# Kernel optimization log

Hardware: AMD Instinct MI355X
Metric: run time of the kernel (lower is better)

## Reference

```python
import jax, jax.numpy as jnp
import numpy as np

N = 50000      # nodes
E = 800000     # edges (avg degree 16)
IN = 64        # input_dim
OUT = 64       # output_dim
T = 4          # num_node_types
R = 5          # num_relations
H = 4          # heads
D = OUT // H   # head_dim = 16
LN_EPS = 1e-5


def setup_inputs() -> dict:
    key = jax.random.key(0)
    ks = jax.random.split(key, 20)
    s = 0.02
    glorot = np.sqrt(6.0 / (D + D))
    inp = {
        "x": jax.random.normal(ks[0], (N, IN), jnp.float32),
        "node_types": jax.random.randint(ks[1], (N,), 0, T, jnp.int32),
        "edge_index": jax.random.randint(ks[2], (2, E), 0, N, jnp.int64),
        "edge_types": jax.random.randint(ks[3], (E,), 0, R, jnp.int32),
        # per-node-type linear layers, stacked: [T, in, out] / [T, out]
        "Wk": jax.random.normal(ks[4], (T, IN, OUT), jnp.float32) * s,
        "bk": jnp.zeros((T, OUT), jnp.float32),
        "Wq": jax.random.normal(ks[5], (T, IN, OUT), jnp.float32) * s,
        "bq": jnp.zeros((T, OUT), jnp.float32),
        "Wv": jax.random.normal(ks[6], (T, IN, OUT), jnp.float32) * s,
        "bv": jnp.zeros((T, OUT), jnp.float32),
        "Wa": jax.random.normal(ks[7], (T, OUT, OUT), jnp.float32) * s,
        "ba": jnp.zeros((T, OUT), jnp.float32),
        # per-node-type LayerNorm params
        "ln_g": jnp.ones((T, OUT), jnp.float32),
        "ln_b": jnp.zeros((T, OUT), jnp.float32),
        # relation params
        "rel_pri": jnp.ones((R, H), jnp.float32),
        "rel_att": jax.random.uniform(ks[8], (R, H, D, D), jnp.float32, -glorot, glorot),
        "rel_msg": jax.random.uniform(ks[9], (R, H, D, D), jnp.float32, -glorot, glorot),
        "skip_weights": jnp.ones((T,), jnp.float32),
    }
    return inp


def _typed_linear(x, W, b, node_types):
    # per-node-type linear: compute all T projections ([T,N,out] is small: T*N*out)
    # then select each node's row by its type.
    all_t = jnp.einsum('ni,tio->tno', x, W)                       # [T,N,out]
    sel = jnp.take_along_axis(all_t, node_types[None, :, None], axis=0)[0]
    return sel + b[node_types]                                     # [N,out]


def _hgt_forward(x, node_types, edge_index, edge_types,
                 Wk, bk, Wq, bq, Wv, bv, Wa, ba, ln_g, ln_b,
                 rel_pri, rel_att, rel_msg, skip_weights):
    src = edge_index[0]   # j (source)
    tgt = edge_index[1]   # i (target, segment id for softmax / aggregation)

    Kn = _typed_linear(x, Wk, bk, node_types)  # [N,out]
    Qn = _typed_linear(x, Wq, bq, node_types)
    Vn = _typed_linear(x, Wv, bv, node_types)

    q = Qn[tgt].reshape(E, H, D)   # [E,H,D]
    k = Kn[src].reshape(E, H, D)
    v = Vn[src].reshape(E, H, D)

    # relation-specific transforms: k' = k @ rel_att[r], v' = v @ rel_msg[r]
    # loop over the small fixed set of relations (avoids [E,H,D,D] gather)
    k2 = jnp.zeros_like(k)
    v2 = jnp.zeros_like(v)
    for r in range(R):
        m = (edge_types == r)[:, None, None]
        k2 = k2 + jnp.where(m, jnp.einsum('ehd,hdf->ehf', k, rel_att[r]), 0.0)
        v2 = v2 + jnp.where(m, jnp.einsum('ehd,hdf->ehf', v, rel_msg[r]), 0.0)

    scale = np.float32(np.sqrt(D))
    att = (q * k2).sum(-1) * rel_pri[edge_types] / scale           # [E,H]

    # segment softmax over edges sharing a target node
    amax = jax.ops.segment_max(att, tgt, num_segments=N)           # [N,H]
    ex = jnp.exp(att - amax[tgt])
    den = jax.ops.segment_sum(ex, tgt, num_segments=N)             # [N,H]
    attw = ex / den[tgt]                                           # [E,H]

    msg = (v2 * attw[..., None]).reshape(E, OUT)                   # [E,out]
    agg = jax.ops.segment_sum(msg, tgt, num_segments=N)            # [N,out]

    # update: gelu -> per-type linear -> skip mix -> per-type LayerNorm
    # (dropout omitted: eval mode)
    out_g = jax.nn.gelu(agg, approximate=False)
    trans = _typed_linear(out_g, Wa, ba, node_types)               # [N,out]
    sk = jax.nn.sigmoid(skip_weights)[node_types][:, None]         # [N,1]
    res = trans * sk + x * (1.0 - sk)
    mu = res.mean(-1, keepdims=True)
    var = res.var(-1, keepdims=True)
    res = (res - mu) / jnp.sqrt(var + LN_EPS)
    return res * ln_g[node_types] + ln_b[node_types]


def reference(x, node_types, edge_index, edge_types,
              Wk, bk, Wq, bq, Wv, bv, Wa, ba, ln_g, ln_b,
              rel_pri, rel_att, rel_msg, skip_weights):
    return _hgt_forward(x, node_types, edge_index, edge_types,
                        Wk, bk, Wq, bq, Wv, bv, Wa, ba, ln_g, ln_b,
                        rel_pri, rel_att, rel_msg, skip_weights)
```

## Files before the change

### kernel.cpp

```cpp
#include <hip/hip_runtime.h>
#include <math.h>

#define N_NODES 50000
#define N_EDGES 800000

#define OFF_KV     0
#define OFF_QN     3200000
#define OFF_AGG    6400000
#define OFF_CNT    9600000
#define OFF_SMALL  10400000
#define OFF_BTH    10400100
#define OFF_ORDER  10401000
#define OFF_COL    10452000

__device__ __forceinline__ float gelu_f(float a) {
    return 0.5f * a * (1.0f + erff(a * 0.70710678118654752f));
}

__device__ __forceinline__ unsigned pack_kv(float kf, float vf) {
    unsigned ku = __float_as_uint(kf);
    ku = (ku + 0x7FFFu + ((ku >> 16) & 1u)) >> 16;
    unsigned vu = __float_as_uint(vf);
    vu = (vu + 0x7FFFu + ((vu >> 16) & 1u)) & 0xFFFF0000u;
    return vu | ku;
}

__global__ __launch_bounds__(256) void scatter_direct_k(const int* __restrict__ ei,
                                                        const int* __restrict__ et,
                                                        const int* __restrict__ ntype,
                                                        int* __restrict__ cnt,
                                                        int* __restrict__ col,
                                                        int* __restrict__ bth) {
    int e = blockIdx.x * 256 + threadIdx.x;
    int tgt = ei[N_EDGES + e];
    int slot = atomicAdd(&cnt[tgt << 4], 1);
    if (slot < 64)
        col[(tgt << 6) + slot] = ei[e] | (et[e] << 20);
    if (blockIdx.x < 196) {
        __shared__ int wc[4][4];
        int tid = threadIdx.x, w = tid >> 6, lane = tid & 63;
        int i = blockIdx.x * 256 + tid;
        int t = (i < N_NODES) ? ntype[i] : 255;
#pragma unroll
        for (int tt = 0; tt < 4; ++tt) {
            unsigned long long m = __ballot(t == tt);
            if (lane == 0) wc[w][tt] = __popcll(m);
        }
        __syncthreads();
        if (tid < 4)
            bth[tid * 196 + blockIdx.x] = wc[0][tid] + wc[1][tid] + wc[2][tid] + wc[3][tid];
    }
}

__global__ __launch_bounds__(256) void typescan_k(int* __restrict__ bth,
                                                  int* __restrict__ small) {
    int tid = threadIdx.x, wv = tid >> 6, lane = tid & 63;
    __shared__ int tot_s[4];
    __shared__ int noff_s[4];
    int pre[4]; int carry = 0;
#pragma unroll
    for (int c = 0; c < 4; ++c) {
        int b = c * 64 + lane;
        int v = (b < 196) ? bth[wv * 196 + b] : 0;
        int s = v;
#pragma unroll
        for (int o = 1; o < 64; o <<= 1) { int u = __shfl_up(s, o); if (lane >= o) s += u; }
        pre[c] = carry + s - v;
        carry += __shfl(s, 63);
    }
    if (lane == 0) tot_s[wv] = carry;
    __syncthreads();
    if (tid == 0) {
        int o = 0, cb = 0;
#pragma unroll
        for (int k = 0; k < 4; ++k) {
            small[k] = tot_s[k];
            small[8 + k] = o; noff_s[k] = o;
            small[16 + k] = cb;
            o += tot_s[k]; cb += (tot_s[k] + 63) >> 6;
        }
        small[12] = o; small[20] = cb;
    }
    __syncthreads();
    int noff = noff_s[wv];
#pragma unroll
    for (int c = 0; c < 4; ++c) {
        int b = c * 64 + lane;
        if (b < 196) bth[wv * 196 + b] = noff + pre[c];
    }
}

__global__ __launch_bounds__(256) void order_k(const int* __restrict__ ntype,
                                               const int* __restrict__ bth,
                                               int* __restrict__ order) {
    int tid = threadIdx.x, w = tid >> 6, lane = tid & 63;
    int i = blockIdx.x * 256 + tid;
    __shared__ int wc[4][4];
    int t = (i < N_NODES) ? ntype[i] : 255;
    int myrank = 0;
#pragma unroll
    for (int tt = 0; tt < 4; ++tt) {
        unsigned long long m = __ballot(t == tt);
        if (lane == 0) wc[w][tt] = __popcll(m);
        if (t == tt) myrank = __popcll(m & ((1ull << lane) - 1ull));
    }
    __syncthreads();
    if (t < 4) {
        int base = 0;
#pragma unroll
        for (int w2 = 0; w2 < 4; ++w2) if (w2 < w) base += wc[w2][t];
        order[bth[t * 196 + blockIdx.x] + base + myrank] = i;
    }
}

__device__ __forceinline__ void mat16(const float* __restrict__ W,
                                      const float* __restrict__ B,
                                      const float* xs, int lane, int wvu,
                                      float acc[16]) {
    const float* Bp = B + wvu * 16;
#pragma unroll
    for (int c = 0; c < 16; c += 4) {
        float4 b4 = *(const float4*)(Bp + c);
        acc[c] = b4.x; acc[c + 1] = b4.y; acc[c + 2] = b4.z; acc[c + 3] = b4.w;
    }
    const float* Wp = W + wvu * 16;
#pragma unroll 4
    for (int i = 0; i < 64; ++i) {
        float xi = xs[i * 64 + lane];
#pragma unroll
        for (int c = 0; c < 16; c += 4) {
            float4 w4 = *(const float4*)(Wp + i * 64 + c);
            acc[c]     = fmaf(xi, w4.x, acc[c]);
            acc[c + 1] = fmaf(xi, w4.y, acc[c + 1]);
            acc[c + 2] = fmaf(xi, w4.z, acc[c + 2]);
            acc[c + 3] = fmaf(xi, w4.w, acc[c + 3]);
        }
    }
}

__global__ __launch_bounds__(256) void kqv_k(const float* __restrict__ x,
                                             const int* __restrict__ order,
                                             const int* __restrict__ small,
                                             const float* __restrict__ Wk, const float* __restrict__ bk,
                                             const float* __restrict__ Wq, const float* __restrict__ bq,
                                             const float* __restrict__ Wv, const float* __restrict__ bv,
                                             float* __restrict__ Qn,
                                             unsigned* __restrict__ KVu) {
    __shared__ float xs[4096];
    int tid = threadIdx.x, wv = tid >> 6, lane = tid & 63;
    int wid = blockIdx.x;
    int cb1 = small[17], cb2 = small[18], cb3 = small[19], cb4 = small[20];
    if (wid >= cb4) return;
    int t = (wid >= cb1) + (wid >= cb2) + (wid >= cb3);
    int cbt = small[16 + t];
    int noff = small[8 + t], cntt = small[t];
    int pos = noff + (wid - cbt) * 64 + lane;
    int end = noff + cntt;
    bool valid = pos < end;
    int node = order[valid ? pos : end - 1];
    t = __builtin_amdgcn_readfirstlane(t);
    int wvu = __builtin_amdgcn_readfirstlane(wv);

    const float* xr = x + node * 64 + wvu * 16;
    float4 a0 = *(const float4*)(xr + 0), a1 = *(const float4*)(xr + 4),
           a2 = *(const float4*)(xr + 8), a3 = *(const float4*)(xr + 12);
    float st[16] = { a0.x, a0.y, a0.z, a0.w, a1.x, a1.y, a1.z, a1.w,
                     a2.x, a2.y, a2.z, a2.w, a3.x, a3.y, a3.z, a3.w };
#pragma unroll
    for (int k = 0; k < 16; ++k) xs[(wvu * 16 + k) * 64 + lane] = st[k];
    __syncthreads();

    float aq[16];
    mat16(Wq + t * 4096, bq + t * 64, xs, lane, wvu, aq);
    if (valid) {
        float* Op = Qn + node * 64 + wvu * 16;
#pragma unroll
        for (int c = 0; c < 16; c += 4) {
            float4 o4 = { aq[c], aq[c + 1], aq[c + 2], aq[c + 3] };
            *(float4*)(Op + c) = o4;
        }
    }
    float ak[16], av[16];
    mat16(Wk + t * 4096, bk + t * 64, xs, lane, wvu, ak);
    mat16(Wv + t * 4096, bv + t * 64, xs, lane, wvu, av);
    if (valid) {
        unsigned pk[16];
#pragma unroll
        for (int c = 0; c < 16; ++c) pk[c] = pack_kv(ak[c], av[c]);
        uint4* dst = (uint4*)(KVu + node * 64 + wvu * 16);
#pragma unroll
        for (int c = 0; c < 4; ++c)
            dst[c] = *(uint4*)&pk[c * 4];
    }
}

#define BF_LO(u) __uint_as_float((u) << 16)
#define BF_HI(u) __uint_as_float((u) & 0xFFFF0000u)

#define LOADB(CC, AA, BB, T) do {                                          \
    int idx_ = (T) * 4 + g; if (idx_ > deg - 1) idx_ = deg - 1;            \
    int cc_ = __shfl(colv, idx_);                                          \
    (CC) = cc_;                                                            \
    const unsigned* kvp_ = KVu + (unsigned)(cc_ & 0xFFFFF) * 64;           \
    (AA) = *(const uint2*)(kvp_ + 2 * l);                                  \
    (BB) = *(const uint2*)(kvp_ + 32 + 2 * l);                             \
} while (0)

#define COMPUTE(CC, AA, BB, T) do {                                        \
    int rr_ = (CC) >> 20;                                                  \
    const float* qq_ = qp_s + rr_ * 64 + 2 * l;                            \
    float2 qA_ = *(const float2*)qq_;                                      \
    float2 qB_ = *(const float2*)(qq_ + 32);                               \
    float kA0_ = BF_LO((AA).x), vA0_ = BF_HI((AA).x);                      \
    float kA1_ = BF_LO((AA).y), vA1_ = BF_HI((AA).y);                      \
    float kB0_ = BF_LO((BB).x), vB0_ = BF_HI((BB).x);                      \
    float kB1_ = BF_LO((BB).y), vB1_ = BF_HI((BB).y);                      \
    float sA_ = fmaf(kA1_, qA_.y, kA0_ * qA_.x);                           \
    float sB_ = fmaf(kB1_, qB_.y, kB0_ * qB_.x);                           \
    sA_ += __shfl_xor(sA_, 1); sB_ += __shfl_xor(sB_, 1);                  \
    sA_ += __shfl_xor(sA_, 2); sB_ += __shfl_xor(sB_, 2);                  \
    sA_ += __shfl_xor(sA_, 4); sB_ += __shfl_xor(sB_, 4);                  \
    bool act_ = ((T) * 4 + g) < deg;                                       \
    float pA_ = act_ ? __expf(sA_) : 0.0f;                                 \
    float pB_ = act_ ? __expf(sB_) : 0.0f;                                 \
    dnA += pA_; dnB += pB_;                                                \
    _Pragma("unroll")                                                      \
    for (int k_ = 0; k_ < 5; ++k_) {                                       \
        bool mk_ = (rr_ == k_);                                            \
        float pAk_ = mk_ ? pA_ : 0.0f, pBk_ = mk_ ? pB_ : 0.0f;            \
        OA[k_].x = fmaf(pAk_, vA0_, OA[k_].x);                             \
        OA[k_].y = fmaf(pAk_, vA1_, OA[k_].y);                             \
        OB[k_].x = fmaf(pBk_, vB0_, OB[k_].x);                             \
        OB[k_].y = fmaf(pBk_, vB1_, OB[k_].y);                             \
    }                                                                      \
} while (0)

__global__ __launch_bounds__(128) void attn_k(const float* __restrict__ Qn,
                                              const unsigned* __restrict__ KVu,
                                              const int* __restrict__ cnt,
                                              const int* __restrict__ col,
                                              const float* __restrict__ rel_att,
                                              const float* __restrict__ rel_msg,
                                              const float* __restrict__ rel_pri,
                                              float* __restrict__ agg) {
    __shared__ float lds[1408];
    const int tid = threadIdx.x, wv = tid >> 6, lane = tid & 63;
    const int g = lane >> 4, l = lane & 15;
    const int node = blockIdx.x * 2 + wv;
    float* q_s  = lds + wv * 704;
    float* qp_s = q_s + 64;
    float* o_s  = qp_s + 320;

    int deg = cnt[node << 4];
    deg = (deg > 64) ? 64 : deg;
    int colv = col[(node << 6) + lane];
    q_s[lane] = Qn[node * 64 + lane];
    __builtin_amdgcn_wave_barrier();

    const int gb = g * 16;
    float4 qf0 = *(const float4*)(q_s + gb + 0);
    float4 qf1 = *(const float4*)(q_s + gb + 4);
    float4 qf2 = *(const float4*)(q_s + gb + 8);
    float4 qf3 = *(const float4*)(q_s + gb + 12);
#pragma unroll
    for (int r = 0; r < 5; ++r) {
        const float* A = rel_att + ((r * 4 + g) * 16 + l) * 16;
        float4 b0 = *(const float4*)(A + 0), b1 = *(const float4*)(A + 4),
               b2 = *(const float4*)(A + 8), b3 = *(const float4*)(A + 12);
        float acc = b0.x * qf0.x;
        acc = fmaf(b0.y, qf0.y, acc); acc = fmaf(b0.z, qf0.z, acc); acc = fmaf(b0.w, qf0.w, acc);
        acc = fmaf(b1.x, qf1.x, acc); acc = fmaf(b1.y, qf1.y, acc);
        acc = fmaf(b1.z, qf1.z, acc); acc = fmaf(b1.w, qf1.w, acc);
        acc = fmaf(b2.x, qf2.x, acc); acc = fmaf(b2.y, qf2.y, acc);
        acc = fmaf(b2.z, qf2.z, acc); acc = fmaf(b2.w, qf2.w, acc);
        acc = fmaf(b3.x, qf3.x, acc); acc = fmaf(b3.y, qf3.y, acc);
        acc = fmaf(b3.z, qf3.z, acc); acc = fmaf(b3.w, qf3.w, acc);
        qp_s[r * 64 + gb + l] = acc * rel_pri[r * 4 + g] * 0.25f;
    }
    __builtin_amdgcn_wave_barrier();

    if (deg == 0) {
        agg[node * 64 + lane] = 0.0f;
        return;
    }
    int nit = (deg + 3) >> 2;

    float dnA = 0.0f, dnB = 0.0f;
    float2 OA[5], OB[5];
#pragma unroll
    for (int k = 0; k < 5; ++k) { OA[k] = {0.f, 0.f}; OB[k] = {0.f, 0.f}; }

    int c0, c1, c2;
    uint2 A0, B0, A1, B1, A2, B2;
    LOADB(c0, A0, B0, 0);
    LOADB(c1, A1, B1, 1);
    LOADB(c2, A2, B2, 2);

    int t = 0;
    for (;;) {
        COMPUTE(c0, A0, B0, t); if (t + 3 < nit) LOADB(c0, A0, B0, t + 3);
        if (++t >= nit) break;
        COMPUTE(c1, A1, B1, t); if (t + 3 < nit) LOADB(c1, A1, B1, t + 3);
        if (++t >= nit) break;
        COMPUTE(c2, A2, B2, t); if (t + 3 < nit) LOADB(c2, A2, B2, t + 3);
        if (++t >= nit) break;
    }

#pragma unroll
    for (int k = 0; k < 5; ++k) {
        OA[k].x += __shfl_xor(OA[k].x, 16); OA[k].x += __shfl_xor(OA[k].x, 32);
        OA[k].y += __shfl_xor(OA[k].y, 16); OA[k].y += __shfl_xor(OA[k].y, 32);
        OB[k].x += __shfl_xor(OB[k].x, 16); OB[k].x += __shfl_xor(OB[k].x, 32);
        OB[k].y += __shfl_xor(OB[k].y, 16); OB[k].y += __shfl_xor(OB[k].y, 32);
    }
    dnA += __shfl_xor(dnA, 16); dnA += __shfl_xor(dnA, 32);
    dnB += __shfl_xor(dnB, 16); dnB += __shfl_xor(dnB, 32);

    if (g == 0) {
#pragma unroll
        for (int k = 0; k < 5; ++k) {
            *(float2*)(o_s + k * 64 + 2 * l) = OA[k];
            *(float2*)(o_s + k * 64 + 32 + 2 * l) = OB[k];
        }
        if (l == 0) { q_s[0] = dnA; q_s[2] = dnB; }
        if (l == 8) { q_s[1] = dnA; q_s[3] = dnB; }
    }
    __builtin_amdgcn_wave_barrier();

    float F = 0.0f;
#pragma unroll
    for (int k = 0; k < 5; ++k) {
        const float* ob = o_s + k * 64 + gb;
        float4 o0 = *(const float4*)(ob + 0), o1 = *(const float4*)(ob + 4),
               o2 = *(const float4*)(ob + 8), o3 = *(const float4*)(ob + 12);
        const float* M = rel_msg + ((k * 4 + g) * 16) * 16 + l;
        F = fmaf(o0.x, M[0],   F); F = fmaf(o0.y, M[16],  F);
        F = fmaf(o0.z, M[32],  F); F = fmaf(o0.w, M[48],  F);
        F = fmaf(o1.x, M[64],  F); F = fmaf(o1.y, M[80],  F);
        F = fmaf(o1.z, M[96],  F); F = fmaf(o1.w, M[112], F);
        F = fmaf(o2.x, M[128], F); F = fmaf(o2.y, M[144], F);
        F = fmaf(o2.z, M[160], F); F = fmaf(o2.w, M[176], F);
        F = fmaf(o3.x, M[192], F); F = fmaf(o3.y, M[208], F);
        F = fmaf(o3.z, M[224], F); F = fmaf(o3.w, M[240], F);
    }
    float dsel = q_s[g];
    float rd = (dsel > 0.0f) ? (1.0f / dsel) : 0.0f;
    agg[node * 64 + lane] = F * rd;
}

__global__ __launch_bounds__(256) void final_k(const float* __restrict__ x,
                                               const int* __restrict__ order,
                                               const int* __restrict__ small,
                                               const float* __restrict__ agg,
                                               const float* __restrict__ Wa,
                                               const float* __restrict__ ba,
                                               const float* __restrict__ ln_g,
                                               const float* __restrict__ ln_b,
                                               const float* __restrict__ skipw,
                                               float* __restrict__ out) {
    __shared__ float xs[4096];
    __shared__ float res_s[4096];
    int tid = threadIdx.x, wv = tid >> 6, lane = tid & 63;
    int wid = blockIdx.x;
    int cb1 = small[17], cb2 = small[18], cb3 = small[19], cb4 = small[20];
    if (wid >= cb4) return;
    int t = (wid >= cb1) + (wid >= cb2) + (wid >= cb3);
    int cbt = small[16 + t];
    int noff = small[8 + t], cntt = small[t];
    int pos = noff + (wid - cbt) * 64 + lane;
    int end = noff + cntt;
    bool valid = pos < end;
    int node = order[valid ? pos : end - 1];
    t = __builtin_amdgcn_readfirstlane(t);
    int wvu = __builtin_amdgcn_readfirstlane(wv);

    const float* ar = agg + node * 64 + wvu * 16;
    float4 a0 = *(const float4*)(ar + 0), a1 = *(const float4*)(ar + 4),
           a2 = *(const float4*)(ar + 8), a3 = *(const float4*)(ar + 12);
    float st[16] = { gelu_f(a0.x), gelu_f(a0.y), gelu_f(a0.z), gelu_f(a0.w),
                     gelu_f(a1.x), gelu_f(a1.y), gelu_f(a1.z), gelu_f(a1.w),
                     gelu_f(a2.x), gelu_f(a2.y), gelu_f(a2.z), gelu_f(a2.w),
                     gelu_f(a3.x), gelu_f(a3.y), gelu_f(a3.z), gelu_f(a3.w) };
#pragma unroll
    for (int k = 0; k < 16; ++k) xs[(wvu * 16 + k) * 64 + lane] = st[k];
    __syncthreads();

    float acc[16];
    const float* Bp = ba + t * 64 + wvu * 16;
#pragma unroll
    for (int c = 0; c < 16; c += 4) {
        float4 b4 = *(const float4*)(Bp + c);
        acc[c] = b4.x; acc[c + 1] = b4.y; acc[c + 2] = b4.z; acc[c + 3] = b4.w;
    }
    const float* Wp = Wa + t * 4096 + wvu * 16;
#pragma unroll 4
    for (int i = 0; i < 64; ++i) {
        float xi = xs[i * 64 + lane];
#pragma unroll
        for (int c = 0; c < 16; c += 4) {
            float4 w4 = *(const float4*)(Wp + i * 64 + c);
            acc[c]     = fmaf(xi, w4.x, acc[c]);
            acc[c + 1] = fmaf(xi, w4.y, acc[c + 1]);
            acc[c + 2] = fmaf(xi, w4.z, acc[c + 2]);
            acc[c + 3] = fmaf(xi, w4.w, acc[c + 3]);
        }
    }
    float sk = 1.0f / (1.0f + __expf(-skipw[t]));
    float om = 1.0f - sk;
    const float* xrow = x + node * 64 + wvu * 16;
#pragma unroll
    for (int c = 0; c < 16; c += 4) {
        float4 xv = *(const float4*)(xrow + c);
        acc[c]     = acc[c] * sk + xv.x * om;
        acc[c + 1] = acc[c + 1] * sk + xv.y * om;
        acc[c + 2] = acc[c + 2] * sk + xv.z * om;
        acc[c + 3] = acc[c + 3] * sk + xv.w * om;
    }
#pragma unroll
    for (int k = 0; k < 16; ++k) res_s[(wvu * 16 + k) * 64 + lane] = acc[k];
    __syncthreads();

    float sum = 0.0f, ssq = 0.0f;
#pragma unroll
    for (int c = 0; c < 64; ++c) {
        float rv = res_s[c * 64 + lane];
        sum += rv; ssq = fmaf(rv, rv, ssq);
    }
    float mu = sum * (1.0f / 64.0f);
    float var = ssq * (1.0f / 64.0f) - mu * mu;
    float rstd = rsqrtf(var + 1e-5f);
    const float* lg = ln_g + t * 64 + wvu * 16;
    const float* lb = ln_b + t * 64 + wvu * 16;
    if (valid) {
        float* op = out + node * 64 + wvu * 16;
#pragma unroll
        for (int c = 0; c < 16; c += 4) {
            float4 ov;
            ov.x = (acc[c]     - mu) * rstd * lg[c]     + lb[c];
            ov.y = (acc[c + 1] - mu) * rstd * lg[c + 1] + lb[c + 1];
            ov.z = (acc[c + 2] - mu) * rstd * lg[c + 2] + lb[c + 2];
            ov.w = (acc[c + 3] - mu) * rstd * lg[c + 3] + lb[c + 3];
            *(float4*)(op + c) = ov;
        }
    }
}

extern "C" void kernel_launch(void* const* d_in, const int* in_sizes, int n_in,
                              void* d_out, int out_size, void* d_ws, size_t ws_size,
                              hipStream_t stream) {
    const float* x       = (const float*)d_in[0];
    const int*   ntype   = (const int*)d_in[1];
    const int*   ei      = (const int*)d_in[2];
    const int*   et      = (const int*)d_in[3];
    const float* Wk      = (const float*)d_in[4];
    const float* bk      = (const float*)d_in[5];
    const float* Wq      = (const float*)d_in[6];
    const float* bq      = (const float*)d_in[7];
    const float* Wv      = (const float*)d_in[8];
    const float* bv      = (const float*)d_in[9];
    const float* Wa      = (const float*)d_in[10];
    const float* ba      = (const float*)d_in[11];
    const float* ln_g    = (const float*)d_in[12];
    const float* ln_b    = (const float*)d_in[13];
    const float* rel_pri = (const float*)d_in[14];
    const float* rel_att = (const float*)d_in[15];
    const float* rel_msg = (const float*)d_in[16];
    const float* skipw   = (const float*)d_in[17];
    float* out = (float*)d_out;

    float* ws = (float*)d_ws;
    unsigned* KVu = (unsigned*)(ws + OFF_KV);
    float* Qn  = ws + OFF_QN;
    float* agg = ws + OFF_AGG;
    int* cnt   = (int*)(ws + OFF_CNT);
    int* small = (int*)(ws + OFF_SMALL);
    int* bth   = (int*)(ws + OFF_BTH);
    int* order = (int*)(ws + OFF_ORDER);
    int* col   = (int*)(ws + OFF_COL);

    hipMemsetAsync(cnt, 0, 800000 * sizeof(int), stream);
    scatter_direct_k<<<3125, 256, 0, stream>>>(ei, et, ntype, cnt, col, bth);
    typescan_k<<<1, 256, 0, stream>>>(bth, small);
    order_k<<<196, 256, 0, stream>>>(ntype, bth, order);
    kqv_k<<<786, 256, 0, stream>>>(x, order, small, Wk, bk, Wq, bq, Wv, bv, Qn, KVu);
    attn_k<<<25000, 128, 0, stream>>>(Qn, KVu, cnt, col, rel_att, rel_msg, rel_pri, agg);
    final_k<<<786, 256, 0, stream>>>(x, order, small, agg, Wa, ba, ln_g, ln_b, skipw, out);
}
```

Before: 223.1 us.

## Fuse edge scatter into KQV kernel and replace memset with prep kernel

Replaces the hipMemsetAsync of the count array with a small prep kernel that zeroes counts and computes per-block type histograms. The edge scatter is moved out of the first kernel and into the KQV projection launch as extra blocks, so the scatter atomics and the projection run concurrently in one grid. This aims to cut launch overhead and let the latency-bound scatter overlap with compute-bound projection work. The fused kernel reserves 16KB of shared memory even in scatter blocks, which can lower their occupancy.

After: 224.5 us. No clear change (+0.6%).

```diff
diff --git a/kernel.cpp b/kernel.cpp
--- a/kernel.cpp
+++ b/kernel.cpp
@@ -13,6 +13,9 @@
 #define OFF_ORDER  10401000
 #define OFF_COL    10452000
 
+#define SCATTER_BLOCKS 3125
+#define KQV_BLOCKS     786
+
 __device__ __forceinline__ float gelu_f(float a) {
     return 0.5f * a * (1.0f + erff(a * 0.70710678118654752f));
 }
@@ -25,31 +28,27 @@
     return vu | ku;
 }
 
-__global__ __launch_bounds__(256) void scatter_direct_k(const int* __restrict__ ei,
-                                                        const int* __restrict__ et,
-                                                        const int* __restrict__ ntype,
-                                                        int* __restrict__ cnt,
-                                                        int* __restrict__ col,
-                                                        int* __restrict__ bth) {
-    int e = blockIdx.x * 256 + threadIdx.x;
-    int tgt = ei[N_EDGES + e];
-    int slot = atomicAdd(&cnt[tgt << 4], 1);
-    if (slot < 64)
-        col[(tgt << 6) + slot] = ei[e] | (et[e] << 20);
-    if (blockIdx.x < 196) {
-        __shared__ int wc[4][4];
-        int tid = threadIdx.x, w = tid >> 6, lane = tid & 63;
-        int i = blockIdx.x * 256 + tid;
-        int t = (i < N_NODES) ? ntype[i] : 255;
-#pragma unroll
-        for (int tt = 0; tt < 4; ++tt) {
-            unsigned long long m = __ballot(t == tt);
-            if (lane == 0) wc[w][tt] = __popcll(m);
-        }
-        __syncthreads();
-        if (tid < 4)
-            bth[tid * 196 + blockIdx.x] = wc[0][tid] + wc[1][tid] + wc[2][tid] + wc[3][tid];
-    }
+__global__ __launch_bounds__(256) void prep_k(const int* __restrict__ ntype,
+                                              int* __restrict__ cnt,
+                                              int* __restrict__ bth) {
+    int tid = threadIdx.x;
+    int i = blockIdx.x * 256 + tid;
+    if (i < N_NODES) {
+        int4 z = {0, 0, 0, 0};
+        int4* p = (int4*)(cnt + i * 16);
+        p[0] = z; p[1] = z; p[2] = z; p[3] = z;
+    }
+    __shared__ int wc[4][4];
+    int w = tid >> 6, lane = tid & 63;
+    int t = (i < N_NODES) ? ntype[i] : 255;
+#pragma unroll
+    for (int tt = 0; tt < 4; ++tt) {
+        unsigned long long m = __ballot(t == tt);
+        if (lane == 0) wc[w][tt] = __popcll(m);
+    }
+    __syncthreads();
+    if (tid < 4)
+        bth[tid * 196 + blockIdx.x] = wc[0][tid] + wc[1][tid] + wc[2][tid] + wc[3][tid];
 }
 
 __global__ __launch_bounds__(256) void typescan_k(int* __restrict__ bth,
@@ -138,17 +137,27 @@
     }
 }
 
-__global__ __launch_bounds__(256) void kqv_k(const float* __restrict__ x,
-                                             const int* __restrict__ order,
-                                             const int* __restrict__ small,
-                                             const float* __restrict__ Wk, const float* __restrict__ bk,
-                                             const float* __restrict__ Wq, const float* __restrict__ bq,
-                                             const float* __restrict__ Wv, const float* __restrict__ bv,
-                                             float* __restrict__ Qn,
-                                             unsigned* __restrict__ KVu) {
+__global__ __launch_bounds__(256) void scatter_kqv_k(
+    const int* __restrict__ ei, const int* __restrict__ et,
+    int* __restrict__ cnt, int* __restrict__ col,
+    const float* __restrict__ x, const int* __restrict__ order,
+    const int* __restrict__ small,
+    const float* __restrict__ Wk, const float* __restrict__ bk,
+    const float* __restrict__ Wq, const float* __restrict__ bq,
+    const float* __restrict__ Wv, const float* __restrict__ bv,
+    float* __restrict__ Qn, unsigned* __restrict__ KVu)
+{
     __shared__ float xs[4096];
+    if (blockIdx.x < SCATTER_BLOCKS) {
+        int e = blockIdx.x * 256 + threadIdx.x;
+        int tgt = ei[N_EDGES + e];
+        int slot = atomicAdd(&cnt[tgt << 4], 1);
+        if (slot < 64)
+            col[(tgt << 6) + slot] = ei[e] | (et[e] << 20);
+        return;
+    }
     int tid = threadIdx.x, wv = tid >> 6, lane = tid & 63;
-    int wid = blockIdx.x;
+    int wid = blockIdx.x - SCATTER_BLOCKS;
     int cb1 = small[17], cb2 = small[18], cb3 = small[19], cb4 = small[20];
     if (wid >= cb4) return;
     int t = (wid >= cb1) + (wid >= cb2) + (wid >= cb3);
@@ -478,11 +487,11 @@
     int* order = (int*)(ws + OFF_ORDER);
     int* col   = (int*)(ws + OFF_COL);
 
-    hipMemsetAsync(cnt, 0, 800000 * sizeof(int), stream);
-    scatter_direct_k<<<3125, 256, 0, stream>>>(ei, et, ntype, cnt, col, bth);
+    prep_k<<<196, 256, 0, stream>>>(ntype, cnt, bth);
     typescan_k<<<1, 256, 0, stream>>>(bth, small);
     order_k<<<196, 256, 0, stream>>>(ntype, bth, order);
-    kqv_k<<<786, 256, 0, stream>>>(x, order, small, Wk, bk, Wq, bq, Wv, bv, Qn, KVu);
+    scatter_kqv_k<<<SCATTER_BLOCKS + KQV_BLOCKS, 256, 0, stream>>>(
+        ei, et, cnt, col, x, order, small, Wk, bk, Wq, bq, Wv, bv, Qn, KVu);
     attn_k<<<25000, 128, 0, stream>>>(Qn, KVu, cnt, col, rel_att, rel_msg, rel_pri, agg);
     final_k<<<786, 256, 0, stream>>>(x, order, small, agg, Wa, ba, ln_g, ln_b, skipw, out);
 }
```
